# Kernel optimization log

Measured on AMD Instinct MI355X. Metric: run time of the kernel, lower is better.

The kernel has to match this reference:

```python
import jax, jax.numpy as jnp
import numpy as np


def setup_inputs() -> dict:
    key = jax.random.key(0)
    k1, k2 = jax.random.split(key)
    B, N, M, C = 32, 4096, 4096, 3
    xyz1 = jax.random.normal(k1, (B, N, C), dtype=jnp.float32)
    xyz2 = jax.random.normal(k2, (B, M, C), dtype=jnp.float32)
    return {"xyz1": xyz1, "xyz2": xyz2}


def _chamfer_l2(xyz1, xyz2):
    # Pairwise squared L2 distances via ||a||^2 + ||b||^2 - 2 a.b  (b n m)
    sq1 = jnp.sum(xyz1 * xyz1, axis=-1)            # [B, N]
    sq2 = jnp.sum(xyz2 * xyz2, axis=-1)            # [B, M]
    cross = jnp.einsum('bnc,bmc->bnm', xyz1, xyz2) # [B, N, M]
    d = sq1[:, :, None] + sq2[:, None, :] - 2.0 * cross
    dist1 = jnp.min(d, axis=2)                     # [B, N] nearest in xyz2
    dist2 = jnp.min(d, axis=1)                     # [B, M] nearest in xyz1
    return jnp.mean(dist1, axis=-1) + jnp.mean(dist2, axis=-1)  # [B]


def reference(xyz1, xyz2):
    return _chamfer_l2(xyz1, xyz2)
```

## Files before the change

kernel.cpp:

```cpp
#include <hip/hip_runtime.h>
#include <hip/hip_bf16.h>

typedef _Float16 half8 __attribute__((ext_vector_type(8)));
typedef float floatx4 __attribute__((ext_vector_type(4)));

#define TPB   256
#define RPTS  1024
#define NT    (RPTS / 16)
#define SMH   (NT * 256)

__global__ __launch_bounds__(TPB, 4) void chamfer_mfma(const float* __restrict__ xyz1,
                                                       const float* __restrict__ xyz2,
                                                       float* __restrict__ out,
                                                       int N, int M) {
    const int b = blockIdx.y, dir = blockIdx.z;
    const float* __restrict__ P = dir ? xyz2 + (size_t)b * M * 3 : xyz1 + (size_t)b * N * 3;
    const float* __restrict__ Q = dir ? xyz1 + (size_t)b * N * 3 : xyz2 + (size_t)b * M * 3;
    const int nq = dir ? M : N;
    const int md = dir ? N : M;

    __shared__ __align__(16) _Float16 smB[SMH + 8];

    const int tid  = (int)threadIdx.x;
    const int w    = tid >> 6;
    const int l    = tid & 63;
    const int m    = l & 15;
    const int quad = l >> 4;

    const _Float16 hz  = (_Float16)0.0f;
    const _Float16 hone = (_Float16)1.0f;

    half8 afr[4];
    float ph[4], valid[4];
    const int qb = blockIdx.x * 256 + w * 64;
#pragma unroll
    for (int g = 0; g < 4; ++g) {
        int idx = qb + g * 16 + m;
        int ci  = idx < nq ? idx : nq - 1;
        float x = P[3 * ci], y = P[3 * ci + 1], z = P[3 * ci + 2];
        ph[g]    = 0.5f * (x * x + y * y + z * z);
        valid[g] = idx < nq ? 1.0f : 0.0f;
        _Float16 xh = (_Float16)x, yh = (_Float16)y, zh = (_Float16)z;
        _Float16 xl = (_Float16)(x - (float)xh);
        _Float16 yl = (_Float16)(y - (float)yh);
        _Float16 zl = (_Float16)(z - (float)zh);
        half8 a;
        if (quad == 0) {
            a[0] = -xh; a[1] = -xh; a[2] = -xl; a[3] = -yh;
            a[4] = -yh; a[5] = -yl; a[6] = -zh; a[7] = -zh;
        } else if (quad == 1) {
            a[0] = -zl; a[1] = hone; a[2] = hone; a[3] = hz;
            a[4] = hz;  a[5] = hz;  a[6] = hz;  a[7] = hz;
        } else {
            a[0] = hz; a[1] = hz; a[2] = hz; a[3] = hz;
            a[4] = hz; a[5] = hz; a[6] = hz; a[7] = hz;
        }
        afr[g] = a;
    }

    float rm[16];
#pragma unroll
    for (int i = 0; i < 16; ++i) rm[i] = 3.0e38f;

    const floatx4 czero = {0.0f, 0.0f, 0.0f, 0.0f};
    const int nrounds = (md + RPTS - 1) / RPTS;

    for (int r = 0; r < nrounds; ++r) {
        if (r) __syncthreads();
#pragma unroll
        for (int k = 0; k < RPTS / TPB; ++k) {
            int j = tid + k * TPB;
            int g = r * RPTS + j;
            g = g < md ? g : md - 1;
            float x = Q[3 * g], y = Q[3 * g + 1], z = Q[3 * g + 2];
            float hq = 0.5f * (x * x + y * y + z * z);
            _Float16 xh = (_Float16)x, yh = (_Float16)y, zh = (_Float16)z;
            _Float16 xl = (_Float16)(x - (float)xh);
            _Float16 yl = (_Float16)(y - (float)yh);
            _Float16 zl = (_Float16)(z - (float)zh);
            _Float16 qh = (_Float16)hq;
            _Float16 ql = (_Float16)(hq - (float)qh);
            int t = j >> 4, c = j & 15;
            half8 v0, v1;
            v0[0] = xh; v0[1] = xl; v0[2] = xh; v0[3] = yh;
            v0[4] = yl; v0[5] = yh; v0[6] = zh; v0[7] = zl;
            v1[0] = zh; v1[1] = qh; v1[2] = ql; v1[3] = hz;
            v1[4] = hz; v1[5] = hz; v1[6] = hz; v1[7] = hz;
            *(half8*)&smB[t * 256 + c * 8]       = v0;
            *(half8*)&smB[t * 256 + 128 + c * 8] = v1;
        }
        if (r == 0 && tid < 8) smB[SMH + tid] = hz;
        __syncthreads();

        const _Float16* bp  = (quad < 2) ? (smB + quad * 128 + m * 8) : (smB + SMH);
        const int       bst = (quad < 2) ? 256 : 0;
        for (int t = 0; t < NT; t += 2) {
            half8 b0 = *(const half8*)bp; bp += bst;
            half8 b1 = *(const half8*)bp; bp += bst;
            floatx4 dA0 = __builtin_amdgcn_mfma_f32_16x16x32_f16(afr[0], b0, czero, 0, 0, 0);
            floatx4 dA1 = __builtin_amdgcn_mfma_f32_16x16x32_f16(afr[1], b0, czero, 0, 0, 0);
            floatx4 dA2 = __builtin_amdgcn_mfma_f32_16x16x32_f16(afr[2], b0, czero, 0, 0, 0);
            floatx4 dA3 = __builtin_amdgcn_mfma_f32_16x16x32_f16(afr[3], b0, czero, 0, 0, 0);
            floatx4 dB0 = __builtin_amdgcn_mfma_f32_16x16x32_f16(afr[0], b1, czero, 0, 0, 0);
            floatx4 dB1 = __builtin_amdgcn_mfma_f32_16x16x32_f16(afr[1], b1, czero, 0, 0, 0);
            floatx4 dB2 = __builtin_amdgcn_mfma_f32_16x16x32_f16(afr[2], b1, czero, 0, 0, 0);
            floatx4 dB3 = __builtin_amdgcn_mfma_f32_16x16x32_f16(afr[3], b1, czero, 0, 0, 0);
#pragma unroll
            for (int i = 0; i < 4; ++i) {
                rm[0 * 4 + i] = fminf(fminf(rm[0 * 4 + i], dA0[i]), dB0[i]);
                rm[1 * 4 + i] = fminf(fminf(rm[1 * 4 + i], dA1[i]), dB1[i]);
                rm[2 * 4 + i] = fminf(fminf(rm[2 * 4 + i], dA2[i]), dB2[i]);
                rm[3 * 4 + i] = fminf(fminf(rm[3 * 4 + i], dA3[i]), dB3[i]);
            }
        }
    }

#pragma unroll
    for (int off = 1; off < 16; off <<= 1) {
#pragma unroll
        for (int i = 0; i < 16; ++i) rm[i] = fminf(rm[i], __shfl_xor(rm[i], off, 64));
    }

    float s = 0.0f;
    if (quad == (m >> 2)) {
        int reg = l & 3;
#pragma unroll
        for (int g = 0; g < 4; ++g) s += valid[g] * (rm[g * 4 + reg] + ph[g]);
    }
#pragma unroll
    for (int off = 32; off > 0; off >>= 1) s += __shfl_down(s, off, 64);
    if (l == 0) atomicAdd(out + b, s * (2.0f / (float)nq));
}

extern "C" void kernel_launch(void* const* d_in, const int* in_sizes, int n_in,
                              void* d_out, int out_size, void* d_ws, size_t ws_size,
                              hipStream_t stream) {
    const float* xyz1 = (const float*)d_in[0];
    const float* xyz2 = (const float*)d_in[1];
    float* out = (float*)d_out;

    const int B = out_size;
    const int N = in_sizes[0] / (3 * B);
    const int M = in_sizes[1] / (3 * B);

    hipMemsetAsync(d_out, 0, (size_t)B * sizeof(float), stream);

    const int qmax = N > M ? N : M;
    dim3 grid((qmax + 255) / 256, B, 2);
    chamfer_mfma<<<grid, dim3(TPB), 0, stream>>>(xyz1, xyz2, out, N, M);
}
```

Measured before the change: 117.2 us.

## Switch distance tiles from 16x16x32 to 32x32x16 MFMA to drop padded lanes

Replaces the 16x16x32 MFMA tiling, where half the K lanes (quads 2-3) carried zero padding, with 32x32x16 MFMA so the 16-wide K packing fills the instruction exactly. The LDS layout becomes 32-point tiles. Each wave now issues 4 larger MFMAs per pair of tiles instead of 8 small ones, and the min-reduction shuffles widen to 32 lanes. It also recomputes the query norms from global memory in the epilogue instead of keeping them in registers, and adds an early exit for out-of-range blocks. The cost is higher register pressure from the 32-entry running-min array and floatx16 accumulators.

```diff
diff --git a/kernel.cpp b/kernel.cpp
--- a/kernel.cpp
+++ b/kernel.cpp
@@ -1,13 +1,12 @@
 #include <hip/hip_runtime.h>
-#include <hip/hip_bf16.h>
 
 typedef _Float16 half8 __attribute__((ext_vector_type(8)));
-typedef float floatx4 __attribute__((ext_vector_type(4)));
+typedef float floatx16 __attribute__((ext_vector_type(16)));
 
 #define TPB   256
 #define RPTS  1024
-#define NT    (RPTS / 16)
-#define SMH   (NT * 256)
+#define NTILE (RPTS / 32)
+#define SMH   (RPTS * 16)
 
 __global__ __launch_bounds__(TPB, 4) void chamfer_mfma(const float* __restrict__ xyz1,
                                                        const float* __restrict__ xyz2,
@@ -19,51 +18,48 @@
     const int nq = dir ? M : N;
     const int md = dir ? N : M;
 
-    __shared__ __align__(16) _Float16 smB[SMH + 8];
+    if ((int)blockIdx.x * TPB >= nq) return;
 
-    const int tid  = (int)threadIdx.x;
-    const int w    = tid >> 6;
-    const int l    = tid & 63;
-    const int m    = l & 15;
-    const int quad = l >> 4;
+    __shared__ __align__(16) _Float16 smB[SMH];
 
-    const _Float16 hz  = (_Float16)0.0f;
-    const _Float16 hone = (_Float16)1.0f;
+    const int tid = (int)threadIdx.x;
+    const int w   = tid >> 6;
+    const int l   = tid & 63;
+    const int m   = l & 31;
+    const int h   = l >> 5;
 
-    half8 afr[4];
-    float ph[4], valid[4];
+    const _Float16 hz = (_Float16)0.0f, hone = (_Float16)1.0f;
     const int qb = blockIdx.x * 256 + w * 64;
+
+    half8 afr[2];
 #pragma unroll
-    for (int g = 0; g < 4; ++g) {
-        int idx = qb + g * 16 + m;
+    for (int g = 0; g < 2; ++g) {
+        int idx = qb + g * 32 + m;
         int ci  = idx < nq ? idx : nq - 1;
         float x = P[3 * ci], y = P[3 * ci + 1], z = P[3 * ci + 2];
-        ph[g]    = 0.5f * (x * x + y * y + z * z);
-        valid[g] = idx < nq ? 1.0f : 0.0f;
         _Float16 xh = (_Float16)x, yh = (_Float16)y, zh = (_Float16)z;
         _Float16 xl = (_Float16)(x - (float)xh);
         _Float16 yl = (_Float16)(y - (float)yh);
         _Float16 zl = (_Float16)(z - (float)zh);
         half8 a;
-        if (quad == 0) {
+        if (h == 0) {
             a[0] = -xh; a[1] = -xh; a[2] = -xl; a[3] = -yh;
             a[4] = -yh; a[5] = -yl; a[6] = -zh; a[7] = -zh;
-        } else if (quad == 1) {
+        } else {
             a[0] = -zl; a[1] = hone; a[2] = hone; a[3] = hz;
-            a[4] = hz;  a[5] = hz;  a[6] = hz;  a[7] = hz;
-        } else {
-            a[0] = hz; a[1] = hz; a[2] = hz; a[3] = hz;
-            a[4] = hz; a[5] = hz; a[6] = hz; a[7] = hz;
+            a[4] = hz;  a[5] = hz;   a[6] = hz;  a[7] = hz;
         }
         afr[g] = a;
     }
 
-    float rm[16];
+    float rm[32];
 #pragma unroll
-    for (int i = 0; i < 16; ++i) rm[i] = 3.0e38f;
+    for (int i = 0; i < 32; ++i) rm[i] = 3.0e38f;
 
-    const floatx4 czero = {0.0f, 0.0f, 0.0f, 0.0f};
+    const floatx16 czero = {0.0f, 0.0f, 0.0f, 0.0f, 0.0f, 0.0f, 0.0f, 0.0f,
+                            0.0f, 0.0f, 0.0f, 0.0f, 0.0f, 0.0f, 0.0f, 0.0f};
     const int nrounds = (md + RPTS - 1) / RPTS;
+    const _Float16* bp = smB + h * 256 + m * 8;
 
     for (int r = 0; r < nrounds; ++r) {
         if (r) __syncthreads();
@@ -80,52 +76,51 @@
             _Float16 zl = (_Float16)(z - (float)zh);
             _Float16 qh = (_Float16)hq;
             _Float16 ql = (_Float16)(hq - (float)qh);
-            int t = j >> 4, c = j & 15;
+            int t = j >> 5, c = j & 31;
             half8 v0, v1;
             v0[0] = xh; v0[1] = xl; v0[2] = xh; v0[3] = yh;
             v0[4] = yl; v0[5] = yh; v0[6] = zh; v0[7] = zl;
             v1[0] = zh; v1[1] = qh; v1[2] = ql; v1[3] = hz;
             v1[4] = hz; v1[5] = hz; v1[6] = hz; v1[7] = hz;
-            *(half8*)&smB[t * 256 + c * 8]       = v0;
-            *(half8*)&smB[t * 256 + 128 + c * 8] = v1;
+            *(half8*)&smB[t * 512 + c * 8]       = v0;
+            *(half8*)&smB[t * 512 + 256 + c * 8] = v1;
         }
-        if (r == 0 && tid < 8) smB[SMH + tid] = hz;
         __syncthreads();
 
-        const _Float16* bp  = (quad < 2) ? (smB + quad * 128 + m * 8) : (smB + SMH);
-        const int       bst = (quad < 2) ? 256 : 0;
-        for (int t = 0; t < NT; t += 2) {
-            half8 b0 = *(const half8*)bp; bp += bst;
-            half8 b1 = *(const half8*)bp; bp += bst;
-            floatx4 dA0 = __builtin_amdgcn_mfma_f32_16x16x32_f16(afr[0], b0, czero, 0, 0, 0);
-            floatx4 dA1 = __builtin_amdgcn_mfma_f32_16x16x32_f16(afr[1], b0, czero, 0, 0, 0);
-            floatx4 dA2 = __builtin_amdgcn_mfma_f32_16x16x32_f16(afr[2], b0, czero, 0, 0, 0);
-            floatx4 dA3 = __builtin_amdgcn_mfma_f32_16x16x32_f16(afr[3], b0, czero, 0, 0, 0);
-            floatx4 dB0 = __builtin_amdgcn_mfma_f32_16x16x32_f16(afr[0], b1, czero, 0, 0, 0);
-            floatx4 dB1 = __builtin_amdgcn_mfma_f32_16x16x32_f16(afr[1], b1, czero, 0, 0, 0);
-            floatx4 dB2 = __builtin_amdgcn_mfma_f32_16x16x32_f16(afr[2], b1, czero, 0, 0, 0);
-            floatx4 dB3 = __builtin_amdgcn_mfma_f32_16x16x32_f16(afr[3], b1, czero, 0, 0, 0);
+        for (int t = 0; t < NTILE; t += 2) {
+            half8 b0 = *(const half8*)(bp + t * 512);
+            half8 b1 = *(const half8*)(bp + t * 512 + 512);
+            floatx16 d0a = __builtin_amdgcn_mfma_f32_32x32x16_f16(afr[0], b0, czero, 0, 0, 0);
+            floatx16 d0b = __builtin_amdgcn_mfma_f32_32x32x16_f16(afr[0], b1, czero, 0, 0, 0);
 #pragma unroll
-            for (int i = 0; i < 4; ++i) {
-                rm[0 * 4 + i] = fminf(fminf(rm[0 * 4 + i], dA0[i]), dB0[i]);
-                rm[1 * 4 + i] = fminf(fminf(rm[1 * 4 + i], dA1[i]), dB1[i]);
-                rm[2 * 4 + i] = fminf(fminf(rm[2 * 4 + i], dA2[i]), dB2[i]);
-                rm[3 * 4 + i] = fminf(fminf(rm[3 * 4 + i], dA3[i]), dB3[i]);
-            }
+            for (int i = 0; i < 16; ++i)
+                rm[i] = fminf(fminf(rm[i], d0a[i]), d0b[i]);
+            floatx16 d1a = __builtin_amdgcn_mfma_f32_32x32x16_f16(afr[1], b0, czero, 0, 0, 0);
+            floatx16 d1b = __builtin_amdgcn_mfma_f32_32x32x16_f16(afr[1], b1, czero, 0, 0, 0);
+#pragma unroll
+            for (int i = 0; i < 16; ++i)
+                rm[16 + i] = fminf(fminf(rm[16 + i], d1a[i]), d1b[i]);
         }
     }
 
 #pragma unroll
-    for (int off = 1; off < 16; off <<= 1) {
+    for (int off = 1; off < 32; off <<= 1) {
 #pragma unroll
-        for (int i = 0; i < 16; ++i) rm[i] = fminf(rm[i], __shfl_xor(rm[i], off, 64));
+        for (int i = 0; i < 32; ++i) rm[i] = fminf(rm[i], __shfl_xor(rm[i], off, 64));
     }
 
     float s = 0.0f;
-    if (quad == (m >> 2)) {
-        int reg = l & 3;
+    if (m < 16) {
+        const int reg = (m & 3) + 4 * (m >> 2);
+        const int row = 4 * h + (m & 3) + 8 * (m >> 2);
 #pragma unroll
-        for (int g = 0; g < 4; ++g) s += valid[g] * (rm[g * 4 + reg] + ph[g]);
+        for (int g = 0; g < 2; ++g) {
+            int idx = qb + g * 32 + row;
+            if (idx < nq) {
+                float x = P[3 * idx], y = P[3 * idx + 1], z = P[3 * idx + 2];
+                s += rm[g * 16 + reg] + 0.5f * (x * x + y * y + z * z);
+            }
+        }
     }
 #pragma unroll
     for (int off = 32; off > 0; off >>= 1) s += __shfl_down(s, off, 64);
```

New measurement: 116.4 us. About the same (-0.6%).
